# Performance work log

Hardware: AMD Instinct MI355X
Metric: run time of the kernel (lower is better)

## Reference

```python
import jax, jax.numpy as jnp
import numpy as np

_MEAN = jnp.array([0.485, 0.456, 0.406], dtype=jnp.float32)
_STD = jnp.array([0.229, 0.224, 0.225], dtype=jnp.float32)
_EPS = 1e-8


def _conv_relu(x, w, b):
    # VGG conv: 3x3, stride 1, pad 1, followed by ReLU. x: [B,C,H,W], w: [O,I,3,3]
    y = jax.lax.conv_general_dilated(x, w, (1, 1), 'SAME',
                                     dimension_numbers=('NCHW', 'OIHW', 'NCHW'))
    return jax.nn.relu(y + b[None, :, None, None])


def _maxpool2(x):
    return jax.lax.reduce_window(x, -jnp.inf, jax.lax.max,
                                 (1, 1, 2, 2), (1, 1, 2, 2), 'VALID')


def _vgg_block3_feats(x, w0, b0, w1, b1, w2, b2, w3, b3, w4, b4, w5, b5, w6, b6):
    # Replicates VGG16.features up to index 15, collecting relu outputs at 11,13,15.
    x = (x - _MEAN[None, :, None, None]) / _STD[None, :, None, None]
    x = _conv_relu(x, w0, b0)            # conv1_1 (idx 0,1)
    x = _conv_relu(x, w1, b1)            # conv1_2 (idx 2,3)
    x = _maxpool2(x)                     # idx 4
    x = _conv_relu(x, w2, b2)            # conv2_1 (idx 5,6)
    x = _conv_relu(x, w3, b3)            # conv2_2 (idx 7,8)
    x = _maxpool2(x)                     # idx 9
    f1 = _conv_relu(x, w4, b4)           # relu after conv3_1 -> idx 11
    f2 = _conv_relu(f1, w5, b5)          # relu after conv3_2 -> idx 13
    f3 = _conv_relu(f2, w6, b6)          # relu after conv3_3 -> idx 15
    # torch.cat([...], dim=1)
    return jnp.concatenate([f1, f2, f3], axis=1)  # [B, 768, H/4, W/4]


def _feat_replace_and_cos_loss(x_feats, s_feats):
    # x_feats, s_feats: [B, C, h, w]. All-pairs cosine NN match across spatial locations.
    B, C, h, w = x_feats.shape
    x_flat = x_feats.reshape(B, C, h * w).transpose(0, 2, 1)   # [B, N, C]
    s_flat = s_feats.reshape(B, C, -1).transpose(0, 2, 1)       # [B, M, C]
    xn = x_flat / (jnp.linalg.norm(x_flat, axis=-1, keepdims=True) + _EPS)
    sn = s_flat / (jnp.linalg.norm(s_flat, axis=-1, keepdims=True) + _EPS)
    sim = jnp.einsum('bnc,bmc->bnm', xn, sn)                    # [B, N, M] (dominant intermediate)
    idx = jnp.argmax(sim, axis=-1)                              # nearest style feature per location
    target = jnp.take_along_axis(s_flat, idx[..., None], axis=1)  # [B, N, C]
    target = jax.lax.stop_gradient(target)                      # styles are under no_grad
    tn = target / (jnp.linalg.norm(target, axis=-1, keepdims=True) + _EPS)
    cos_d = jnp.sum(xn * tn, axis=-1)                           # cosine sim along channel dim
    return jnp.mean(1.0 - cos_d)


def setup_inputs() -> dict:
    key = jax.random.key(0)
    ks = jax.random.split(key, 16)
    outputs = jax.random.uniform(ks[0], (4, 3, 256, 256), dtype=jnp.float32)
    styles = jax.random.uniform(ks[1], (4, 3, 256, 256), dtype=jnp.float32)
    # VGG16 conv stack up to conv3_3 (OIHW), He-scaled random weights
    chans = [(64, 3), (64, 64), (128, 64), (128, 128), (256, 128), (256, 256), (256, 256)]
    inp = {'outputs': outputs, 'styles': styles}
    for i, (o, c) in enumerate(chans):
        std = float(np.sqrt(2.0 / (c * 9)))
        inp[f'w{i}'] = jax.random.normal(ks[2 + 2 * i], (o, c, 3, 3), dtype=jnp.float32) * std
        inp[f'b{i}'] = jnp.zeros((o,), dtype=jnp.float32)
    return inp


def reference(outputs, styles, w0, b0, w1, b1, w2, b2, w3, b3, w4, b4, w5, b5, w6, b6):
    params = (w0, b0, w1, b1, w2, b2, w3, b3, w4, b4, w5, b5, w6, b6)
    x_feats = _vgg_block3_feats(outputs, *params)
    s_feats = jax.lax.stop_gradient(_vgg_block3_feats(styles, *params))  # with torch.no_grad()
    nn_loss = _feat_replace_and_cos_loss(x_feats, s_feats)
    return nn_loss
```

## Files before the change

### kernel.cpp

```cpp
#include <hip/hip_runtime.h>
#include <hip/hip_bf16.h>

__constant__ float c_mean[3] = {0.485f, 0.456f, 0.406f};
__constant__ float c_istd[3] = {1.0f/0.229f, 1.0f/0.224f, 1.0f/0.225f};

typedef __attribute__((ext_vector_type(8))) short short8;
typedef __attribute__((ext_vector_type(4))) float floatv4;
typedef unsigned short ushort;

__device__ inline float bf2f(ushort u) {
  unsigned int x = ((unsigned int)u) << 16;
  float f; __builtin_memcpy(&f, &x, 4); return f;
}
__device__ inline ushort f2bf(float f) {
  __hip_bfloat16 h = __float2bfloat16(f);
  ushort u; __builtin_memcpy(&u, &h, 2); return u;
}

__global__ __launch_bounds__(256) void zero_k(float* __restrict__ p, int n)
{
  int i = blockIdx.x * 256 + threadIdx.x;
  if (i < n) p[i] = 0.f;
}

__global__ __launch_bounds__(256) void wtrans_k(const float* __restrict__ w,
                                                ushort* __restrict__ Wp,
                                                int OC, int IC)
{
  int t = blockIdx.x * 256 + threadIdx.x;
  int total = OC * IC * 9;
  if (t >= total) return;
  int oct16 = OC >> 4;
  int j = t & 7;
  int L = (t >> 3) & 63;
  int f = t >> 9;
  int ot = f % oct16;
  int r  = f / oct16;
  int tap = r % 9;
  int kc  = r / 9;
  int oc = ot * 16 + (L & 15);
  int ic = kc * 32 + ((L >> 4) << 3) + j;
  Wp[(size_t)f * 512 + L * 8 + j] = f2bf(w[((size_t)oc * IC + ic) * 9 + tap]);
}

__global__ __launch_bounds__(256) void conv0_k(const float* __restrict__ imgA,
                                               const float* __restrict__ imgB,
                                               const float* __restrict__ w,
                                               const float* __restrict__ bias,
                                               ushort* __restrict__ Yh)
{
  __shared__ float wl[27][64];
  __shared__ float bl[64];
  const int tid = threadIdx.x;
  for (int i = tid; i < 1728; i += 256) {
    int o = i & 63, t = i >> 6;
    wl[t][o] = w[o * 27 + t];
  }
  if (tid < 64) bl[tid] = bias[tid];
  __syncthreads();
  int px = blockIdx.x * 256 + tid;
  int b = px >> 16, rem = px & 65535;
  int y = rem >> 8, x = rem & 255;
  const float* img = (b < 4) ? (imgA + (size_t)b * 3 * 65536)
                             : (imgB + (size_t)(b - 4) * 3 * 65536);
  float iv[27];
#pragma unroll
  for (int c = 0; c < 3; ++c)
#pragma unroll
    for (int dy = 0; dy < 3; ++dy)
#pragma unroll
      for (int dx = 0; dx < 3; ++dx) {
        int gy = y - 1 + dy, gx = x - 1 + dx;
        float v = 0.f;
        if (gy >= 0 && gy < 256 && gx >= 0 && gx < 256)
          v = (img[(size_t)c * 65536 + gy * 256 + gx] - c_mean[c]) * c_istd[c];
        iv[c * 9 + dy * 3 + dx] = v;
      }
  float acc[64];
#pragma unroll
  for (int o = 0; o < 64; ++o) acc[o] = 0.f;
#pragma unroll
  for (int t = 0; t < 27; ++t) {
    float v = iv[t];
#pragma unroll
    for (int o = 0; o < 64; ++o) acc[o] = fmaf(v, wl[t][o], acc[o]);
  }
  size_t base = (size_t)px * 64;
#pragma unroll
  for (int o8 = 0; o8 < 8; ++o8) {
    short8 vh;
#pragma unroll
    for (int j = 0; j < 8; ++j)
      vh[j] = (short)f2bf(fmaxf(acc[o8 * 8 + j] + bl[o8 * 8 + j], 0.f));
    *(short8*)(Yh + base + o8 * 8) = vh;
  }
}

template<int TH, int WPY, int WPO, bool POOL, bool SSQ, bool TIN, bool TOUT>
__global__ __launch_bounds__(256) void convmf_k(
    const ushort* __restrict__ Xh,
    const ushort* __restrict__ Wp,
    const float* __restrict__ bias,
    ushort* __restrict__ Yh,
    float* __restrict__ ssq,
    int H, int W, int IC, int in_stride, int ic_off,
    int OC, int out_stride, int oc_off, int octiles)
{
  constexpr int HR = TH + 2;
  constexpr int HALO = HR * 18;
  constexpr int OCB = WPO * 64;
  __shared__ ushort xs_h[4 * HALO * 8];

  const int tid = threadIdx.x;
  const int wave = tid >> 6, lane = tid & 63;
  const int quad = lane >> 4, l16 = lane & 15;
  const int wy = wave / WPO, wo = wave % WPO;
  const int bb = blockIdx.z / octiles, ot = blockIdx.z % octiles;
  const int y0 = blockIdx.y * TH, x0 = blockIdx.x * 16;
  const int ocbase = ot * OCB + wo * 64;
  const int oct16 = OC >> 4;

  floatv4 acc[4][4];
#pragma unroll
  for (int tn = 0; tn < 4; ++tn)
#pragma unroll
    for (int tm = 0; tm < 4; ++tm) acc[tn][tm] = (floatv4){0.f, 0.f, 0.f, 0.f};

  for (int k0 = 0; k0 < IC; k0 += 32) {
    __syncthreads();
    for (int u = tid; u < HALO * 4; u += 256) {
      int px = u >> 2, icq = u & 3;
      int hy = px / 18, hx = px - hy * 18;
      int gy = y0 - 1 + hy, gx = x0 - 1 + hx;
      int4 vh = {0, 0, 0, 0};
      if (gy >= 0 && gy < H && gx >= 0 && gx < W) {
        size_t g;
        if (TIN) {
          int kc = (ic_off + k0 + icq * 8) >> 3;
          g = (((size_t)(bb * ((H * W) >> 4) + gy * (W >> 4) + (gx >> 4)) * (in_stride >> 3) + kc) << 7)
              + ((gx & 15) << 3);
        } else {
          g = ((size_t)(bb * H + gy) * W + gx) * in_stride + ic_off + k0 + icq * 8;
        }
        vh = *(const int4*)(Xh + g);
      }
      *(int4*)&xs_h[(icq * HALO + px) * 8] = vh;
    }
    __syncthreads();

#pragma unroll
    for (int tap = 0; tap < 9; ++tap) {
      const int dy = tap / 3, dx = tap % 3;
      const size_t wg = (((size_t)(k0 >> 5) * 9 + tap) * oct16 + (ocbase >> 4)) * 512 + (size_t)lane * 8;
      short8 bh[4];
#pragma unroll
      for (int tm = 0; tm < 4; ++tm)
        bh[tm] = *(const short8*)(Wp + wg + tm * 512);
#pragma unroll
      for (int tn = 0; tn < 4; ++tn) {
        int p = wy * 64 + tn * 16 + l16;
        int ty = p >> 4, tx = p & 15;
        int hp = (ty + dy) * 18 + tx + dx;
        short8 ah = *(const short8*)&xs_h[(quad * HALO + hp) * 8];
#pragma unroll
        for (int tm = 0; tm < 4; ++tm)
          acc[tn][tm] = __builtin_amdgcn_mfma_f32_16x16x32_bf16(ah, bh[tm], acc[tn][tm], 0, 0, 0);
      }
    }
  }

  if (POOL) {
    const int oH = H >> 1, oW = W >> 1;
#pragma unroll
    for (int tm = 0; tm < 4; ++tm) {
      int ocg = ocbase + tm * 16 + l16;
      float bv = bias[ocg];
#pragma unroll
      for (int tn2 = 0; tn2 < 2; ++tn2)
#pragma unroll
        for (int r2 = 0; r2 < 2; ++r2) {
          float v0 = fmaxf(acc[2 * tn2][tm][2 * r2]     + bv, 0.f);
          float v1 = fmaxf(acc[2 * tn2][tm][2 * r2 + 1] + bv, 0.f);
          float v2 = fmaxf(acc[2 * tn2 + 1][tm][2 * r2]     + bv, 0.f);
          float v3 = fmaxf(acc[2 * tn2 + 1][tm][2 * r2 + 1] + bv, 0.f);
          float v = fmaxf(fmaxf(v0, v1), fmaxf(v2, v3));
          int oy = (y0 >> 1) + wy * 2 + tn2;
          int ox = (x0 >> 1) + quad * 2 + r2;
          Yh[((size_t)(bb * oH + oy) * oW + ox) * out_stride + oc_off + ocg] = f2bf(v);
        }
    }
  } else {
    float sv[4][4];
    if (SSQ) {
#pragma unroll
      for (int tn = 0; tn < 4; ++tn)
#pragma unroll
        for (int r = 0; r < 4; ++r) sv[tn][r] = 0.f;
    }
#pragma unroll
    for (int tm = 0; tm < 4; ++tm) {
      int ocg = ocbase + tm * 16 + l16;
      float bv = bias[ocg];
#pragma unroll
      for (int tn = 0; tn < 4; ++tn)
#pragma unroll
        for (int r = 0; r < 4; ++r) {
          int p = wy * 64 + tn * 16 + quad * 4 + r;
          int ty = p >> 4, tx = p & 15;
          float v = fmaxf(acc[tn][tm][r] + bv, 0.f);
          ushort h = f2bf(v);
          if (SSQ) { float vr = bf2f(h); sv[tn][r] = fmaf(vr, vr, sv[tn][r]); }
          size_t o;
          if (TOUT) {
            int n_out = (y0 + ty) * W + x0 + tx;
            int oc = oc_off + ocg;
            o = (((size_t)(bb * ((H * W) >> 4) + (n_out >> 4)) * (out_stride >> 3) + (oc >> 3)) << 7)
                + ((n_out & 15) << 3) + (oc & 7);
          } else {
            o = ((size_t)(bb * H + y0 + ty) * W + x0 + tx) * out_stride + oc_off + ocg;
          }
          Yh[o] = h;
        }
    }
    if (SSQ) {
#pragma unroll
      for (int tn = 0; tn < 4; ++tn)
#pragma unroll
        for (int r = 0; r < 4; ++r) {
          float s = sv[tn][r];
          s += __shfl_xor(s, 1, 64);
          s += __shfl_xor(s, 2, 64);
          s += __shfl_xor(s, 4, 64);
          s += __shfl_xor(s, 8, 64);
          if (l16 == 0) {
            int p = wy * 64 + tn * 16 + quad * 4 + r;
            int ty = p >> 4, tx = p & 15;
            atomicAdd(&ssq[(size_t)bb * 4096 + (y0 + ty) * 64 + x0 + tx], s);
          }
        }
    }
  }
}

__global__ __launch_bounds__(256) void finalize_k(float* __restrict__ p, int n)
{
  int i = blockIdx.x * 256 + threadIdx.x;
  if (i < n) p[i] = 1.0f / (sqrtf(p[i]) + 1e-8f);
}

__global__ __launch_bounds__(256) void simmax_k(
    const ushort* __restrict__ Ct,
    const float* __restrict__ invns, float* __restrict__ partial)
{
  __shared__ float redbuf[2][128];
  const int tid = threadIdx.x;
  const int lane = tid & 63, wave = tid >> 6;
  const int quad = lane >> 4, l16 = lane & 15;
  const int wn0 = (wave >> 1) * 64;
  const int wm0 = (wave & 1) * 64;
  const int n0 = blockIdx.x * 128;
  const int ms = blockIdx.y;
  const int b  = blockIdx.z;

  float runmax[4][4];
#pragma unroll
  for (int tn = 0; tn < 4; ++tn)
#pragma unroll
    for (int r = 0; r < 4; ++r) runmax[tn][r] = -1e30f;

  const ushort* xbase = Ct + (((size_t)(b * 256 + (n0 >> 4) + (wn0 >> 4)) * 96) << 7) + ((size_t)l16 << 3);

  for (int mc = 0; mc < 4; ++mc) {
    const ushort* sbase = Ct + (((size_t)((b + 4) * 256 + ms * 32 + mc * 8 + (wm0 >> 4)) * 96) << 7) + ((size_t)l16 << 3);
    floatv4 acc[4][4];
#pragma unroll
    for (int tn = 0; tn < 4; ++tn)
#pragma unroll
      for (int tm = 0; tm < 4; ++tm) acc[tn][tm] = (floatv4){0.f, 0.f, 0.f, 0.f};

#pragma unroll 2
    for (int kc0 = 0; kc0 < 96; kc0 += 4) {
      short8 ah[4], bh[4];
#pragma unroll
      for (int t = 0; t < 4; ++t)
        ah[t] = *(const short8*)(xbase + (((size_t)t * 96 + kc0 + quad) << 7));
#pragma unroll
      for (int t = 0; t < 4; ++t)
        bh[t] = *(const short8*)(sbase + (((size_t)t * 96 + kc0 + quad) << 7));
#pragma unroll
      for (int tn = 0; tn < 4; ++tn)
#pragma unroll
        for (int tm = 0; tm < 4; ++tm)
          acc[tn][tm] = __builtin_amdgcn_mfma_f32_16x16x32_bf16(ah[tn], bh[tm], acc[tn][tm], 0, 0, 0);
    }

    const int m0 = ms * 512 + mc * 128;
#pragma unroll
    for (int tm = 0; tm < 4; ++tm) {
      float inv = invns[(size_t)b * 4096 + m0 + wm0 + tm * 16 + l16];
#pragma unroll
      for (int tn = 0; tn < 4; ++tn)
#pragma unroll
        for (int r = 0; r < 4; ++r)
          runmax[tn][r] = fmaxf(runmax[tn][r], acc[tn][tm][r] * inv);
    }
  }

#pragma unroll
  for (int off = 1; off < 16; off <<= 1)
#pragma unroll
    for (int tn = 0; tn < 4; ++tn)
#pragma unroll
      for (int r = 0; r < 4; ++r)
        runmax[tn][r] = fmaxf(runmax[tn][r], __shfl_xor(runmax[tn][r], off, 64));

  if (l16 == 0) {
#pragma unroll
    for (int tn = 0; tn < 4; ++tn)
#pragma unroll
      for (int r = 0; r < 4; ++r)
        redbuf[wave & 1][wn0 + tn * 16 + quad * 4 + r] = runmax[tn][r];
  }
  __syncthreads();
  if (tid < 128) {
    float mx = fmaxf(redbuf[0][tid], redbuf[1][tid]);
    partial[((size_t)ms * 4 + b) * 4096 + n0 + tid] = mx;
  }
}

__global__ __launch_bounds__(256) void loss_k(const float* __restrict__ partial,
                                              const float* __restrict__ invnx,
                                              float* __restrict__ out)
{
  float sum = 0.f;
  for (int i = threadIdx.x; i < 16384; i += 256) {
    float mx = partial[i];
#pragma unroll
    for (int j = 1; j < 8; ++j) mx = fmaxf(mx, partial[j * 16384 + i]);
    sum += mx * invnx[i];
  }
  __shared__ float red[256];
  red[threadIdx.x] = sum;
  __syncthreads();
  for (int s = 128; s > 0; s >>= 1) {
    if (threadIdx.x < s) red[threadIdx.x] += red[threadIdx.x + s];
    __syncthreads();
  }
  if (threadIdx.x == 0) out[0] = 1.f - red[0] * (1.f / 16384.f);
}

extern "C" void kernel_launch(void* const* d_in, const int* in_sizes, int n_in,
                              void* d_out, int out_size, void* d_ws, size_t ws_size,
                              hipStream_t stream)
{
  const float* outputs = (const float*)d_in[0];
  const float* styles  = (const float*)d_in[1];
  const float* w[7]; const float* bs[7];
  for (int i = 0; i < 7; ++i) { w[i] = (const float*)d_in[2 + 2 * i]; bs[i] = (const float*)d_in[3 + 2 * i]; }

  ushort* p = (ushort*)d_ws;
  ushort* A_h = p; p += 33554432;
  ushort* B_h = p; p += 8388608;
  ushort* cat_h = p; p += 25165824;
  ushort* W1p = p; p += 36864;
  ushort* W2p = p; p += 73728;
  ushort* W3p = p; p += 147456;
  ushort* W4p = p; p += 294912;
  ushort* W5p = p; p += 589824;
  ushort* W6p = p; p += 589824;
  float* nrm = (float*)p;
  float* partial = nrm + 32768;

  zero_k<<<dim3(128), 256, 0, stream>>>(nrm, 32768);

  wtrans_k<<<dim3((9*64*64   + 255)/256), 256, 0, stream>>>(w[1], W1p, 64, 64);
  wtrans_k<<<dim3((9*128*64  + 255)/256), 256, 0, stream>>>(w[2], W2p, 128, 64);
  wtrans_k<<<dim3((9*128*128 + 255)/256), 256, 0, stream>>>(w[3], W3p, 128, 128);
  wtrans_k<<<dim3((9*256*128 + 255)/256), 256, 0, stream>>>(w[4], W4p, 256, 128);
  wtrans_k<<<dim3((9*256*256 + 255)/256), 256, 0, stream>>>(w[5], W5p, 256, 256);
  wtrans_k<<<dim3((9*256*256 + 255)/256), 256, 0, stream>>>(w[6], W6p, 256, 256);

  conv0_k<<<dim3(2048), 256, 0, stream>>>(outputs, styles, w[0], bs[0], A_h);
  convmf_k<16,4,1,true,false,false,false><<<dim3(16,16,8), 256, 0, stream>>>(A_h, W1p, bs[1],
      B_h, nullptr, 256,256, 64, 64,0, 64, 64,0, 1);
  convmf_k<16,4,1,false,false,false,false><<<dim3(8,8,16), 256, 0, stream>>>(B_h, W2p, bs[2],
      A_h, nullptr, 128,128, 64, 64,0, 128, 128,0, 2);
  convmf_k<16,4,1,true,false,false,false><<<dim3(8,8,16), 256, 0, stream>>>(A_h, W3p, bs[3],
      B_h, nullptr, 128,128, 128, 128,0, 128, 128,0, 2);
  convmf_k<16,4,1,false,true,false,true><<<dim3(4,4,32), 256, 0, stream>>>(B_h, W4p, bs[4],
      cat_h, nrm, 64,64, 128, 128,0, 256, 768,0, 4);
  convmf_k<16,4,1,false,true,true,true><<<dim3(4,4,32), 256, 0, stream>>>(cat_h, W5p, bs[5],
      cat_h, nrm, 64,64, 256, 768,0, 256, 768,256, 4);
  convmf_k<16,4,1,false,true,true,true><<<dim3(4,4,32), 256, 0, stream>>>(cat_h, W6p, bs[6],
      cat_h, nrm, 64,64, 256, 768,256, 256, 768,512, 4);

  finalize_k<<<dim3(128), 256, 0, stream>>>(nrm, 32768);

  simmax_k<<<dim3(32, 8, 4), 256, 0, stream>>>(cat_h, nrm + 16384, partial);
  loss_k<<<dim3(1), 256, 0, stream>>>(partial, nrm, (float*)d_out);
}
```

Baseline: 564.7 us.

## Double-buffer conv halo via direct global-to-LDS loads and merge small launches

The conv kernel now stages its input halo with global_load_lds into two LDS buffers, so the next channel chunk is fetched while MFMAs run on the current one. Per-slot address pointers are precomputed once, and out-of-bounds slots read from a zeroed page instead of branching. The LDS layout becomes pixel-major with quads interleaved. The six weight-transform launches are merged into one, the finalize kernel is folded into simmax and loss as inline rsqrt-style math, and the simmax grid axes are swapped. This cuts launch overhead and exposed load latency, at the cost of doubled LDS use, which may lower occupancy.

```diff
diff --git a/kernel.cpp b/kernel.cpp
--- a/kernel.cpp
+++ b/kernel.cpp
@@ -1,5 +1,8 @@
 #include <hip/hip_runtime.h>
 #include <hip/hip_bf16.h>
+
+#define AS1 __attribute__((address_space(1)))
+#define AS3 __attribute__((address_space(3)))
 
 __constant__ float c_mean[3] = {0.485f, 0.456f, 0.406f};
 __constant__ float c_istd[3] = {1.0f/0.229f, 1.0f/0.224f, 1.0f/0.225f};
@@ -23,11 +26,8 @@
   if (i < n) p[i] = 0.f;
 }
 
-__global__ __launch_bounds__(256) void wtrans_k(const float* __restrict__ w,
-                                                ushort* __restrict__ Wp,
-                                                int OC, int IC)
-{
-  int t = blockIdx.x * 256 + threadIdx.x;
+__device__ inline void wtr(const float* w, ushort* Wp, int OC, int IC, int t)
+{
   int total = OC * IC * 9;
   if (t >= total) return;
   int oct16 = OC >> 4;
@@ -43,6 +43,21 @@
   Wp[(size_t)f * 512 + L * 8 + j] = f2bf(w[((size_t)oc * IC + ic) * 9 + tap]);
 }
 
+__global__ __launch_bounds__(256) void wtrans_all_k(
+    const float* w1, const float* w2, const float* w3,
+    const float* w4, const float* w5, const float* w6,
+    ushort* W1, ushort* W2, ushort* W3, ushort* W4, ushort* W5, ushort* W6)
+{
+  int blk = blockIdx.x;
+  int tid = threadIdx.x;
+  if      (blk < 144)  wtr(w1, W1, 64,  64,  blk * 256 + tid);
+  else if (blk < 432)  wtr(w2, W2, 128, 64,  (blk - 144) * 256 + tid);
+  else if (blk < 1008) wtr(w3, W3, 128, 128, (blk - 432) * 256 + tid);
+  else if (blk < 2160) wtr(w4, W4, 256, 128, (blk - 1008) * 256 + tid);
+  else if (blk < 4464) wtr(w5, W5, 256, 256, (blk - 2160) * 256 + tid);
+  else                 wtr(w6, W6, 256, 256, (blk - 4464) * 256 + tid);
+}
+
 __global__ __launch_bounds__(256) void conv0_k(const float* __restrict__ imgA,
                                                const float* __restrict__ imgB,
                                                const float* __restrict__ w,
@@ -103,13 +118,15 @@
     const float* __restrict__ bias,
     ushort* __restrict__ Yh,
     float* __restrict__ ssq,
+    const ushort* __restrict__ zpage,
     int H, int W, int IC, int in_stride, int ic_off,
     int OC, int out_stride, int oc_off, int octiles)
 {
   constexpr int HR = TH + 2;
   constexpr int HALO = HR * 18;
-  constexpr int OCB = WPO * 64;
-  __shared__ ushort xs_h[4 * HALO * 8];
+  constexpr int NJ = (HALO * 4 + 255) / 256;
+  constexpr int SLOTS = NJ * 256;
+  __shared__ ushort xs[2][SLOTS * 8];
 
   const int tid = threadIdx.x;
   const int wave = tid >> 6, lane = tid & 63;
@@ -117,36 +134,55 @@
   const int wy = wave / WPO, wo = wave % WPO;
   const int bb = blockIdx.z / octiles, ot = blockIdx.z % octiles;
   const int y0 = blockIdx.y * TH, x0 = blockIdx.x * 16;
-  const int ocbase = ot * OCB + wo * 64;
+  const int ocbase = ot * (WPO * 64) + wo * 64;
   const int oct16 = OC >> 4;
 
+  const ushort* gb[NJ];
+  int stp[NJ];
+#pragma unroll
+  for (int j = 0; j < NJ; ++j) {
+    int u = tid + j * 256;
+    int px = u >> 2, icq = u & 3;
+    int hy = px / 18, hx = px - hy * 18;
+    int gy = y0 - 1 + hy, gx = x0 - 1 + hx;
+    bool valid = (gy >= 0 && gy < H && gx >= 0 && gx < W);
+    int cgy = valid ? gy : 0, cgx = valid ? gx : 0;
+    size_t g0;
+    if (TIN) {
+      int tile = bb * ((H * W) >> 4) + cgy * (W >> 4) + (cgx >> 4);
+      g0 = (((size_t)tile * (in_stride >> 3) + (ic_off >> 3) + icq) << 7) + ((cgx & 15) << 3);
+    } else {
+      g0 = ((size_t)(bb * H + cgy) * W + cgx) * in_stride + ic_off + icq * 8;
+    }
+    gb[j]  = valid ? (Xh + g0) : zpage;
+    stp[j] = valid ? (TIN ? 16 : 1) : 0;
+  }
+
   floatv4 acc[4][4];
 #pragma unroll
   for (int tn = 0; tn < 4; ++tn)
 #pragma unroll
     for (int tm = 0; tm < 4; ++tm) acc[tn][tm] = (floatv4){0.f, 0.f, 0.f, 0.f};
 
-  for (int k0 = 0; k0 < IC; k0 += 32) {
+  const int NC = IC >> 5;
+
+#pragma unroll
+  for (int j = 0; j < NJ; ++j)
+    __builtin_amdgcn_global_load_lds((AS1 const void*)gb[j],
+        (AS3 void*)&xs[0][(size_t)(tid + j * 256) * 8], 16, 0, 0);
+
+  for (int ci = 0; ci < NC; ++ci) {
     __syncthreads();
-    for (int u = tid; u < HALO * 4; u += 256) {
-      int px = u >> 2, icq = u & 3;
-      int hy = px / 18, hx = px - hy * 18;
-      int gy = y0 - 1 + hy, gx = x0 - 1 + hx;
-      int4 vh = {0, 0, 0, 0};
-      if (gy >= 0 && gy < H && gx >= 0 && gx < W) {
-        size_t g;
-        if (TIN) {
-          int kc = (ic_off + k0 + icq * 8) >> 3;
-          g = (((size_t)(bb * ((H * W) >> 4) + gy * (W >> 4) + (gx >> 4)) * (in_stride >> 3) + kc) << 7)
-              + ((gx & 15) << 3);
-        } else {
-          g = ((size_t)(bb * H + gy) * W + gx) * in_stride + ic_off + k0 + icq * 8;
-        }
-        vh = *(const int4*)(Xh + g);
-      }
-      *(int4*)&xs_h[(icq * HALO + px) * 8] = vh;
-    }
-    __syncthreads();
+    if (ci + 1 < NC) {
+      const int k0n = (ci + 1) * 32;
+      const int nbuf = (ci + 1) & 1;
+#pragma unroll
+      for (int j = 0; j < NJ; ++j)
+        __builtin_amdgcn_global_load_lds((AS1 const void*)(gb[j] + (size_t)k0n * stp[j]),
+            (AS3 void*)&xs[nbuf][(size_t)(tid + j * 256) * 8], 16, 0, 0);
+    }
+    const ushort* xsc = xs[ci & 1];
+    const int k0 = ci * 32;
 
 #pragma unroll
     for (int tap = 0; tap < 9; ++tap) {
@@ -161,7 +197,7 @@
         int p = wy * 64 + tn * 16 + l16;
         int ty = p >> 4, tx = p & 15;
         int hp = (ty + dy) * 18 + tx + dx;
-        short8 ah = *(const short8*)&xs_h[(quad * HALO + hp) * 8];
+        short8 ah = *(const short8*)&xsc[(size_t)(hp * 4 + quad) * 8];
 #pragma unroll
         for (int tm = 0; tm < 4; ++tm)
           acc[tn][tm] = __builtin_amdgcn_mfma_f32_16x16x32_bf16(ah, bh[tm], acc[tn][tm], 0, 0, 0);
@@ -242,15 +278,9 @@
   }
 }
 
-__global__ __launch_bounds__(256) void finalize_k(float* __restrict__ p, int n)
-{
-  int i = blockIdx.x * 256 + threadIdx.x;
-  if (i < n) p[i] = 1.0f / (sqrtf(p[i]) + 1e-8f);
-}
-
 __global__ __launch_bounds__(256) void simmax_k(
     const ushort* __restrict__ Ct,
-    const float* __restrict__ invns, float* __restrict__ partial)
+    const float* __restrict__ ssqs, float* __restrict__ partial)
 {
   __shared__ float redbuf[2][128];
   const int tid = threadIdx.x;
@@ -258,8 +288,8 @@
   const int quad = lane >> 4, l16 = lane & 15;
   const int wn0 = (wave >> 1) * 64;
   const int wm0 = (wave & 1) * 64;
-  const int n0 = blockIdx.x * 128;
-  const int ms = blockIdx.y;
+  const int ms = blockIdx.x;
+  const int n0 = blockIdx.y * 128;
   const int b  = blockIdx.z;
 
   float runmax[4][4];
@@ -297,7 +327,8 @@
     const int m0 = ms * 512 + mc * 128;
 #pragma unroll
     for (int tm = 0; tm < 4; ++tm) {
-      float inv = invns[(size_t)b * 4096 + m0 + wm0 + tm * 16 + l16];
+      float sq = ssqs[(size_t)b * 4096 + m0 + wm0 + tm * 16 + l16];
+      float inv = 1.0f / (sqrtf(sq) + 1e-8f);
 #pragma unroll
       for (int tn = 0; tn < 4; ++tn)
 #pragma unroll
@@ -329,7 +360,7 @@
 }
 
 __global__ __launch_bounds__(256) void loss_k(const float* __restrict__ partial,
-                                              const float* __restrict__ invnx,
+                                              const float* __restrict__ ssqx,
                                               float* __restrict__ out)
 {
   float sum = 0.f;
@@ -337,7 +368,7 @@
     float mx = partial[i];
 #pragma unroll
     for (int j = 1; j < 8; ++j) mx = fmaxf(mx, partial[j * 16384 + i]);
-    sum += mx * invnx[i];
+    sum += mx * (1.0f / (sqrtf(ssqx[i]) + 1e-8f));
   }
   __shared__ float red[256];
   red[threadIdx.x] = sum;
@@ -369,33 +400,28 @@
   ushort* W5p = p; p += 589824;
   ushort* W6p = p; p += 589824;
   float* nrm = (float*)p;
-  float* partial = nrm + 32768;
-
-  zero_k<<<dim3(128), 256, 0, stream>>>(nrm, 32768);
-
-  wtrans_k<<<dim3((9*64*64   + 255)/256), 256, 0, stream>>>(w[1], W1p, 64, 64);
-  wtrans_k<<<dim3((9*128*64  + 255)/256), 256, 0, stream>>>(w[2], W2p, 128, 64);
-  wtrans_k<<<dim3((9*128*128 + 255)/256), 256, 0, stream>>>(w[3], W3p, 128, 128);
-  wtrans_k<<<dim3((9*256*128 + 255)/256), 256, 0, stream>>>(w[4], W4p, 256, 128);
-  wtrans_k<<<dim3((9*256*256 + 255)/256), 256, 0, stream>>>(w[5], W5p, 256, 256);
-  wtrans_k<<<dim3((9*256*256 + 255)/256), 256, 0, stream>>>(w[6], W6p, 256, 256);
+  float* zpage = nrm + 32768;
+  float* partial = zpage + 1024;
+
+  zero_k<<<dim3(132), 256, 0, stream>>>(nrm, 33792);
+
+  wtrans_all_k<<<dim3(6768), 256, 0, stream>>>(w[1], w[2], w[3], w[4], w[5], w[6],
+                                               W1p, W2p, W3p, W4p, W5p, W6p);
 
   conv0_k<<<dim3(2048), 256, 0, stream>>>(outputs, styles, w[0], bs[0], A_h);
   convmf_k<16,4,1,true,false,false,false><<<dim3(16,16,8), 256, 0, stream>>>(A_h, W1p, bs[1],
-      B_h, nullptr, 256,256, 64, 64,0, 64, 64,0, 1);
+      B_h, nullptr, (const ushort*)zpage, 256,256, 64, 64,0, 64, 64,0, 1);
   convmf_k<16,4,1,false,false,false,false><<<dim3(8,8,16), 256, 0, stream>>>(B_h, W2p, bs[2],
-      A_h, nullptr, 128,128, 64, 64,0, 128, 128,0, 2);
+      A_h, nullptr, (const ushort*)zpage, 128,128, 64, 64,0, 128, 128,0, 2);
   convmf_k<16,4,1,true,false,false,false><<<dim3(8,8,16), 256, 0, stream>>>(A_h, W3p, bs[3],
-      B_h, nullptr, 128,128, 128, 128,0, 128, 128,0, 2);
+      B_h, nullptr, (const ushort*)zpage, 128,128, 128, 128,0, 128, 128,0, 2);
   convmf_k<16,4,1,false,true,false,true><<<dim3(4,4,32), 256, 0, stream>>>(B_h, W4p, bs[4],
-      cat_h, nrm, 64,64, 128, 128,0, 256, 768,0, 4);
+      cat_h, nrm, (const ushort*)zpage, 64,64, 128, 128,0, 256, 768,0, 4);
   convmf_k<16,4,1,false,true,true,true><<<dim3(4,4,32), 256, 0, stream>>>(cat_h, W5p, bs[5],
-      cat_h, nrm, 64,64, 256, 768,0, 256, 768,256, 4);
+      cat_h, nrm, (const ushort*)zpage, 64,64, 256, 768,0, 256, 768,256, 4);
   convmf_k<16,4,1,false,true,true,true><<<dim3(4,4,32), 256, 0, stream>>>(cat_h, W6p, bs[6],
-      cat_h, nrm, 64,64, 256, 768,256, 256, 768,512, 4);
-
-  finalize_k<<<dim3(128), 256, 0, stream>>>(nrm, 32768);
-
-  simmax_k<<<dim3(32, 8, 4), 256, 0, stream>>>(cat_h, nrm + 16384, partial);
+      cat_h, nrm, (const ushort*)zpage, 64,64, 256, 768,256, 256, 768,512, 4);
+
+  simmax_k<<<dim3(8, 32, 4), 256, 0, stream>>>(cat_h, nrm + 16384, partial);
   loss_k<<<dim3(1), 256, 0, stream>>>(partial, nrm, (float*)d_out);
 }
```

After: 548.2 us. 1.03x faster.
